# Kernel tuning notes

Measured on AMD Instinct MI355X. Metric: run time of the kernel, lower is better.

The kernel has to match this reference:

```python
import jax, jax.numpy as jnp
import numpy as np

KERNEL_SIZE = 6
PAD = (KERNEL_SIZE - 2) // 4  # 1


def _polyphase(k1d):
    # torch: flip(k.reshape(-1,2).permute(1,0), dims=(1,)) -> (2, K/2)
    # row 0 = even-index taps reversed, row 1 = odd-index taps reversed
    return jnp.flip(k1d.reshape(-1, 2).T, axis=1)


def _upfir_last(x, f):
    """Polyphase synthesis along last axis.
    x: (..., N), f: (2, K2). Pads reflect by PAD, correlates with each
    polyphase filter (stride-1 cross-correlation as in F.conv2d), then
    interleaves the two outputs -> (..., 2N). Even outputs come from f[0].
    """
    N = x.shape[-1]
    K2 = f.shape[1]
    pad_cfg = [(0, 0)] * (x.ndim - 1) + [(PAD, PAD)]
    xp = jnp.pad(x, pad_cfg, mode='reflect')  # (..., N + 2*PAD), N+2*PAD-K2+1 == N
    y0 = sum(f[0, j] * xp[..., j:j + N] for j in range(K2))
    y1 = sum(f[1, j] * xp[..., j:j + N] for j in range(K2))
    return jnp.stack([y0, y1], axis=-1).reshape(*x.shape[:-1], 2 * N)


def _upfir_rows(x, f):
    # synthesis along axis -2 (the H axis); matches torch's .mT transpose dance
    return jnp.swapaxes(_upfir_last(jnp.swapaxes(x, -1, -2), f), -1, -2)


def setup_inputs() -> dict:
    key = jax.random.key(0)
    ks = jax.random.split(key, 6)
    B, C, H, W = 4, 64, 256, 256
    return {
        'ss': jax.random.normal(ks[0], (B, C, H, W), dtype=jnp.float32),
        'sd': jax.random.normal(ks[1], (B, C, H, W), dtype=jnp.float32),
        'ds': jax.random.normal(ks[2], (B, C, H, W), dtype=jnp.float32),
        'dd': jax.random.normal(ks[3], (B, C, H, W), dtype=jnp.float32),
        'h': jax.random.normal(ks[4], (KERNEL_SIZE,), dtype=jnp.float32),
        'g': jax.random.normal(ks[5], (KERNEL_SIZE,), dtype=jnp.float32),
    }


def reference(ss, sd, ds, dd, h, g):
    # single level inverse 2D DWT (levels=1, normalize_approximation=False)
    fh = _polyphase(h)
    fg = _polyphase(g)
    # columns pass (along H): reconstruct low-pass rows `s` and high-pass rows `d`
    s = _upfir_rows(ss, fh) + _upfir_rows(sd, fg)  # (B,C,2H,W)
    d = _upfir_rows(ds, fh) + _upfir_rows(dd, fg)  # (B,C,2H,W)
    # rows pass (along W)
    out = _upfir_last(s, fh) + _upfir_last(d, fg)  # (B,C,2H,2W)
    return out
```

## Files before the change

kernel.cpp:

```cpp
#include <hip/hip_runtime.h>


typedef float float4v __attribute__((ext_vector_type(4)));

constexpr int Hc = 256;
constexpr int Wc = 256;
constexpr int ROWS = 8;
constexpr int WPB  = 4;

__global__ __launch_bounds__(256) void idwt_kernel(
    const float* __restrict__ ss, const float* __restrict__ sd,
    const float* __restrict__ ds, const float* __restrict__ dd,
    const float* __restrict__ hf, const float* __restrict__ gf,
    float* __restrict__ out)
{
    const int lane = threadIdx.x;
    const int wid  = threadIdx.y;
    const int i0   = (blockIdx.x * WPB + wid) * ROWS;
    const int bc   = blockIdx.y;

    const float h0 = hf[0], h1 = hf[1], h2 = hf[2];
    const float h3 = hf[3], h4 = hf[4], h5 = hf[5];
    const float g0 = gf[0], g1 = gf[1], g2 = gf[2];
    const float g3 = gf[3], g4 = gf[4], g5 = gf[5];

    const size_t off = (size_t)bc * (Hc * Wc);
    const int j0 = lane * 4;
    const float* pss = ss + off + j0;
    const float* psd = sd + off + j0;
    const float* pds = ds + off + j0;
    const float* pdd = dd + off + j0;

    auto ld = [&](const float* p, int r) -> float4v {
        return *reinterpret_cast<const float4v*>(p + (size_t)r * Wc);
    };

    const int rm = (i0 == 0) ? 1 : i0 - 1;
    float4v s_m = ld(pss, rm), s_c = ld(pss, i0), s_p = ld(pss, i0 + 1);
    float4v t_m = ld(psd, rm), t_c = ld(psd, i0), t_p = ld(psd, i0 + 1);
    float4v u_m = ld(pds, rm), u_c = ld(pds, i0), u_p = ld(pds, i0 + 1);
    float4v v_m = ld(pdd, rm), v_c = ld(pdd, i0), v_p = ld(pdd, i0 + 1);

    const int W2 = 2 * Wc;
    float* obase = out + (size_t)bc * (2 * Hc) * W2 + 8 * lane;

    auto left = [&](const float4v& w) -> float {
        float l = __shfl_up(w[3], 1);
        return (lane == 0) ? w[1] : l;
    };
    auto right = [&](const float4v& w) -> float {
        float rr = __shfl_down(w[0], 1);
        return (lane == 63) ? w[2] : rr;
    };

    #pragma unroll
    for (int r = 0; r < ROWS; ++r) {
        const int i  = i0 + r;

        const int ip = (i + 2 < Hc) ? i + 2 : Hc - 2;
        const float4v s_f = ld(pss, ip);
        const float4v t_f = ld(psd, ip);
        const float4v u_f = ld(pds, ip);
        const float4v v_f = ld(pdd, ip);

        float4v vs0, vs1, vd0, vd1;
        #pragma unroll
        for (int k = 0; k < 4; ++k) {
            vs0[k] = h4*s_m[k] + h2*s_c[k] + h0*s_p[k] + g4*t_m[k] + g2*t_c[k] + g0*t_p[k];
            vs1[k] = h5*s_m[k] + h3*s_c[k] + h1*s_p[k] + g5*t_m[k] + g3*t_c[k] + g1*t_p[k];
            vd0[k] = h4*u_m[k] + h2*u_c[k] + h0*u_p[k] + g4*v_m[k] + g2*v_c[k] + g0*v_p[k];
            vd1[k] = h5*u_m[k] + h3*u_c[k] + h1*u_p[k] + g5*v_m[k] + g3*v_c[k] + g1*v_p[k];
        }

        const float a [6] = { left(vs0), vs0[0], vs0[1], vs0[2], vs0[3], right(vs0) };
        const float b [6] = { left(vd0), vd0[0], vd0[1], vd0[2], vd0[3], right(vd0) };
        const float c2[6] = { left(vs1), vs1[0], vs1[1], vs1[2], vs1[3], right(vs1) };
        const float d2[6] = { left(vd1), vd1[0], vd1[1], vd1[2], vd1[3], right(vd1) };

        float4v o00, o01, o10, o11;
        #pragma unroll
        for (int t = 0; t < 4; ++t) {
            const float e0 = h4*a [t] + h2*a [t+1] + h0*a [t+2] + g4*b [t] + g2*b [t+1] + g0*b [t+2];
            const float e1 = h5*a [t] + h3*a [t+1] + h1*a [t+2] + g5*b [t] + g3*b [t+1] + g1*b [t+2];
            const float f0 = h4*c2[t] + h2*c2[t+1] + h0*c2[t+2] + g4*d2[t] + g2*d2[t+1] + g0*d2[t+2];
            const float f1 = h5*c2[t] + h3*c2[t+1] + h1*c2[t+2] + g5*d2[t] + g3*d2[t+1] + g1*d2[t+2];
            if (t < 2) {
                o00[2*t]     = e0; o00[2*t+1]     = e1;
                o10[2*t]     = f0; o10[2*t+1]     = f1;
            } else {
                o01[2*(t-2)] = e0; o01[2*(t-2)+1] = e1;
                o11[2*(t-2)] = f0; o11[2*(t-2)+1] = f1;
            }
        }

        float* orow0 = obase + (size_t)(2 * i) * W2;
        float* orow1 = orow0 + W2;
        *reinterpret_cast<float4v*>(orow0)     = o00;
        *reinterpret_cast<float4v*>(orow0 + 4) = o01;
        *reinterpret_cast<float4v*>(orow1)     = o10;
        *reinterpret_cast<float4v*>(orow1 + 4) = o11;

        s_m = s_c; s_c = s_p; s_p = s_f;
        t_m = t_c; t_c = t_p; t_p = t_f;
        u_m = u_c; u_c = u_p; u_p = u_f;
        v_m = v_c; v_c = v_p; v_p = v_f;
    }
}

extern "C" void kernel_launch(void* const* d_in, const int* in_sizes, int n_in,
                              void* d_out, int out_size, void* d_ws, size_t ws_size,
                              hipStream_t stream) {
    const float* ss = (const float*)d_in[0];
    const float* sd = (const float*)d_in[1];
    const float* ds = (const float*)d_in[2];
    const float* dd = (const float*)d_in[3];
    const float* hf = (const float*)d_in[4];
    const float* gf = (const float*)d_in[5];
    float* out = (float*)d_out;

    const int BC = in_sizes[0] / (Hc * Wc);
    dim3 block(64, WPB);
    dim3 grid(Hc / (ROWS * WPB), BC);
    idwt_kernel<<<grid, block, 0, stream>>>(ss, sd, ds, dd, hf, gf, out);
}
```

Measured before the change: 455.9 us.

## Stage input row tiles through LDS with one input stream per wave

Each block now covers 8 output row pairs instead of 32. Each of its four waves loads one input subband (ss, sd, ds, dd) for 10 rows, halo included, into shared memory. After a barrier, each wave computes two row pairs by reading all four streams from LDS. This spreads the global loads across waves and issues them all up front to raise memory-level parallelism. The cost is more halo reloads (10 rows per 8 instead of 34 per 32), 40 KB of LDS per block that may limit occupancy, and a sync.

```diff
diff --git a/kernel.cpp b/kernel.cpp
--- a/kernel.cpp
+++ b/kernel.cpp
@@ -6,7 +6,7 @@
 constexpr int Hc = 256;
 constexpr int Wc = 256;
 constexpr int ROWS = 8;
-constexpr int WPB  = 4;
+constexpr int NS   = ROWS + 2;
 
 __global__ __launch_bounds__(256) void idwt_kernel(
     const float* __restrict__ ss, const float* __restrict__ sd,
@@ -16,8 +16,10 @@
 {
     const int lane = threadIdx.x;
     const int wid  = threadIdx.y;
-    const int i0   = (blockIdx.x * WPB + wid) * ROWS;
+    const int i0   = blockIdx.x * ROWS;
     const int bc   = blockIdx.y;
+
+    __shared__ float lds[4][NS][Wc];
 
     const float h0 = hf[0], h1 = hf[1], h2 = hf[2];
     const float h3 = hf[3], h4 = hf[4], h5 = hf[5];
@@ -25,21 +27,25 @@
     const float g3 = gf[3], g4 = gf[4], g5 = gf[5];
 
     const size_t off = (size_t)bc * (Hc * Wc);
-    const int j0 = lane * 4;
-    const float* pss = ss + off + j0;
-    const float* psd = sd + off + j0;
-    const float* pds = ds + off + j0;
-    const float* pdd = dd + off + j0;
 
-    auto ld = [&](const float* p, int r) -> float4v {
-        return *reinterpret_cast<const float4v*>(p + (size_t)r * Wc);
-    };
+    const float* sbase =
+        (wid == 0 ? ss : wid == 1 ? sd : wid == 2 ? ds : dd) + off + 4 * lane;
 
     const int rm = (i0 == 0) ? 1 : i0 - 1;
-    float4v s_m = ld(pss, rm), s_c = ld(pss, i0), s_p = ld(pss, i0 + 1);
-    float4v t_m = ld(psd, rm), t_c = ld(psd, i0), t_p = ld(psd, i0 + 1);
-    float4v u_m = ld(pds, rm), u_c = ld(pds, i0), u_p = ld(pds, i0 + 1);
-    float4v v_m = ld(pdd, rm), v_c = ld(pdd, i0), v_p = ld(pdd, i0 + 1);
+    const int rp = (i0 + ROWS < Hc) ? i0 + ROWS : Hc - 2;
+
+    float4v stg[NS];
+    stg[0] = *reinterpret_cast<const float4v*>(sbase + (size_t)rm * Wc);
+    #pragma unroll
+    for (int k = 0; k < ROWS; ++k)
+        stg[1 + k] = *reinterpret_cast<const float4v*>(sbase + (size_t)(i0 + k) * Wc);
+    stg[NS - 1] = *reinterpret_cast<const float4v*>(sbase + (size_t)rp * Wc);
+
+    #pragma unroll
+    for (int s = 0; s < NS; ++s)
+        *reinterpret_cast<float4v*>(&lds[wid][s][4 * lane]) = stg[s];
+
+    __syncthreads();
 
     const int W2 = 2 * Wc;
     float* obase = out + (size_t)bc * (2 * Hc) * W2 + 8 * lane;
@@ -52,24 +58,27 @@
         float rr = __shfl_down(w[0], 1);
         return (lane == 63) ? w[2] : rr;
     };
+    auto ldsrow = [&](int stream, int slot) -> float4v {
+        return *reinterpret_cast<const float4v*>(&lds[stream][slot][4 * lane]);
+    };
 
     #pragma unroll
-    for (int r = 0; r < ROWS; ++r) {
-        const int i  = i0 + r;
+    for (int rr = 0; rr < 2; ++rr) {
+        const int local = 2 * wid + rr;
+        const int i = i0 + local;
 
-        const int ip = (i + 2 < Hc) ? i + 2 : Hc - 2;
-        const float4v s_f = ld(pss, ip);
-        const float4v t_f = ld(psd, ip);
-        const float4v u_f = ld(pds, ip);
-        const float4v v_f = ld(pdd, ip);
+        const float4v Sm = ldsrow(0, local), Sc = ldsrow(0, local + 1), Sp = ldsrow(0, local + 2);
+        const float4v Tm = ldsrow(1, local), Tc = ldsrow(1, local + 1), Tp = ldsrow(1, local + 2);
+        const float4v Um = ldsrow(2, local), Uc = ldsrow(2, local + 1), Up = ldsrow(2, local + 2);
+        const float4v Vm = ldsrow(3, local), Vc = ldsrow(3, local + 1), Vp = ldsrow(3, local + 2);
 
         float4v vs0, vs1, vd0, vd1;
         #pragma unroll
         for (int k = 0; k < 4; ++k) {
-            vs0[k] = h4*s_m[k] + h2*s_c[k] + h0*s_p[k] + g4*t_m[k] + g2*t_c[k] + g0*t_p[k];
-            vs1[k] = h5*s_m[k] + h3*s_c[k] + h1*s_p[k] + g5*t_m[k] + g3*t_c[k] + g1*t_p[k];
-            vd0[k] = h4*u_m[k] + h2*u_c[k] + h0*u_p[k] + g4*v_m[k] + g2*v_c[k] + g0*v_p[k];
-            vd1[k] = h5*u_m[k] + h3*u_c[k] + h1*u_p[k] + g5*v_m[k] + g3*v_c[k] + g1*v_p[k];
+            vs0[k] = h4*Sm[k] + h2*Sc[k] + h0*Sp[k] + g4*Tm[k] + g2*Tc[k] + g0*Tp[k];
+            vs1[k] = h5*Sm[k] + h3*Sc[k] + h1*Sp[k] + g5*Tm[k] + g3*Tc[k] + g1*Tp[k];
+            vd0[k] = h4*Um[k] + h2*Uc[k] + h0*Up[k] + g4*Vm[k] + g2*Vc[k] + g0*Vp[k];
+            vd1[k] = h5*Um[k] + h3*Uc[k] + h1*Up[k] + g5*Vm[k] + g3*Vc[k] + g1*Vp[k];
         }
 
         const float a [6] = { left(vs0), vs0[0], vs0[1], vs0[2], vs0[3], right(vs0) };
@@ -99,11 +108,6 @@
         *reinterpret_cast<float4v*>(orow0 + 4) = o01;
         *reinterpret_cast<float4v*>(orow1)     = o10;
         *reinterpret_cast<float4v*>(orow1 + 4) = o11;
-
-        s_m = s_c; s_c = s_p; s_p = s_f;
-        t_m = t_c; t_c = t_p; t_p = t_f;
-        u_m = u_c; u_c = u_p; u_p = u_f;
-        v_m = v_c; v_c = v_p; v_p = v_f;
     }
 }
 
@@ -119,7 +123,7 @@
     float* out = (float*)d_out;
 
     const int BC = in_sizes[0] / (Hc * Wc);
-    dim3 block(64, WPB);
-    dim3 grid(Hc / (ROWS * WPB), BC);
+    dim3 block(64, 4);
+    dim3 grid(Hc / ROWS, BC);
     idwt_kernel<<<grid, block, 0, stream>>>(ss, sd, ds, dd, hf, gf, out);
 }
```

Result: faster. 439.4 us (-3.6%).
